# Kernel tuning notes

Measured on AMD Instinct MI355X. Metric: run time of the kernel, lower is better.

Reference implementation:

```python
import jax, jax.numpy as jnp
import numpy as np

B, D, P, C = 256, 2048, 8192, 8
N_CLUSTERS = P // C
MOMENTUM, TEMP = 0.2, 0.07
NEG_INF = jnp.float32(-1e30)


def setup_inputs() -> dict:
    key = jax.random.key(0)
    k1, k2, k3 = jax.random.split(key, 3)
    batch_feat = jax.random.normal(k1, (B, D), dtype=jnp.float32)
    batch_feat = batch_feat / jnp.linalg.norm(batch_feat, axis=1, keepdims=True)
    memory = jax.random.normal(k2, (P, D), dtype=jnp.float32)
    memory = memory / jnp.linalg.norm(memory, axis=1, keepdims=True)
    abs_proxy_label = jax.random.randint(k3, (B,), 0, P, dtype=jnp.int32)
    # each proxy is a (camera, cluster) pair: proxy p -> cam p % C, cluster p // C
    proxy_cam = (jnp.arange(P, dtype=jnp.int32) % C)
    proxy_cluster = (jnp.arange(P, dtype=jnp.int32) // C)
    camid = abs_proxy_label % C               # consistent with mapper[cam]
    pseudo_cluster_label = abs_proxy_label // C
    return dict(batch_feat=batch_feat, memory=memory,
                abs_proxy_label=abs_proxy_label, camid=camid,
                pseudo_cluster_label=pseudo_cluster_label,
                proxy_cam=proxy_cam, proxy_cluster=proxy_cluster,
                epoch=10, inter_loss_epoch=5, k=50)


def reference(batch_feat, memory, abs_proxy_label, camid, pseudo_cluster_label,
              proxy_cam, proxy_cluster, epoch, inter_loss_epoch, k):
    # ---------------- intra-camera proxy loss ----------------
    sim = (batch_feat @ memory.T) / TEMP                      # [B, P]
    cam_mask = camid[:, None] == proxy_cam[None, :]           # per-cam proxy subset
    logits = jnp.where(cam_mask, sim, NEG_INF)
    lse = jax.nn.logsumexp(logits, axis=1)
    tgt = jnp.take_along_axis(logits, abs_proxy_label[:, None].astype(jnp.int32), axis=1)[:, 0]
    ce = lse - tgt                                            # per-sample CE over its cam's proxies
    ones = jnp.ones((B,), dtype=jnp.float32)
    cam_counts = jax.ops.segment_sum(ones, camid, num_segments=C)
    ce_per_cam = jax.ops.segment_sum(ce, camid, num_segments=C)
    intra_loss = jnp.sum(jnp.where(cam_counts > 0, ce_per_cam / jnp.maximum(cam_counts, 1.0), 0.0))

    loss = intra_loss
    # ---------------- inter-camera loss ----------------
    if epoch >= inter_loss_epoch:
        sim_det = jax.lax.stop_gradient(batch_feat) @ memory.T     # kNN uses detached feat, no temp
        pos_mask = (proxy_cluster[None, :] == pseudo_cluster_label[:, None]) & \
                   (proxy_cam[None, :] != camid[:, None])          # same cluster, different cam
        neg_mask = proxy_cluster[None, :] != pseudo_cluster_label[:, None]  # inlier, different cluster
        neg_sim = jnp.where(neg_mask, sim_det, NEG_INF)
        thresh = jax.lax.top_k(neg_sim, k)[0][:, -1]               # drop k nearest negatives
        keep_neg = neg_mask & (sim_det < thresh[:, None])
        full_mask = pos_mask | keep_neg
        inter_logits = jnp.where(full_mask, sim, NEG_INF)
        logsm = inter_logits - jax.nn.logsumexp(inter_logits, axis=1, keepdims=True)
        pos_card = jnp.sum(pos_mask, axis=1).astype(jnp.float32)
        pos_sum = jnp.sum(jnp.where(pos_mask, logsm, 0.0), axis=1)
        loss_i = jnp.where(pos_card > 0, -pos_sum / jnp.maximum(pos_card, 1.0), 0.0)
        inter_per_cam = jax.ops.segment_sum(loss_i, camid, num_segments=C)
        loss = loss + jnp.sum(jnp.where(cam_counts > 0,
                                        0.5 * inter_per_cam / jnp.maximum(cam_counts, 1.0), 0.0))

    # ---------------- EMA memory-bank scatter update (torch does this in backward) ----------------
    def step(mem, xy):
        x, y = xy
        m = MOMENTUM * mem[y] + (1.0 - MOMENTUM) * x
        m = m / jnp.linalg.norm(m)
        return mem.at[y].set(m), None
    new_memory, _ = jax.lax.scan(
        step, memory, (jax.lax.stop_gradient(batch_feat), abs_proxy_label))
    return loss, new_memory
```

## Files before the change

### kernel.cpp

```cpp
#include <hip/hip_runtime.h>
#include <cstdint>

#define NB 256
#define ND 2048
#define NP 8192
#define NEG_INF_F (-1e30f)
#define INV_TEMP (1.0f/0.07f)

typedef __attribute__((ext_vector_type(8))) short          short8;
typedef __attribute__((ext_vector_type(8))) unsigned short ushort8;
typedef __attribute__((ext_vector_type(4))) float          floatx4;

__device__ __forceinline__ unsigned short f2bf(float f) {
  unsigned u = __float_as_uint(f);
  return (unsigned short)((u + 0x7fffu + ((u >> 16) & 1u)) >> 16);
}

__global__ __launch_bounds__(256)
void prep_kernel(const float* __restrict__ mem, const float* __restrict__ feat,
                 unsigned short* __restrict__ Mb, unsigned short* __restrict__ Fb,
                 float* __restrict__ memcopy ,
                 float* __restrict__ acc, unsigned* __restrict__ counter) {
  const int b = blockIdx.x, t = threadIdx.x;
  if (b < 8192) {
    const float4* src = (const float4*)(mem + (size_t)b * ND) + 2 * t;
    float4 a = src[0], c = src[1];
    ushort8 r;
    r[0]=f2bf(a.x); r[1]=f2bf(a.y); r[2]=f2bf(a.z); r[3]=f2bf(a.w);
    r[4]=f2bf(c.x); r[5]=f2bf(c.y); r[6]=f2bf(c.z); r[7]=f2bf(c.w);
    *(ushort8*)(Mb + (size_t)b * ND + 8 * t) = r;
    float* dst = memcopy + (size_t)b * ND + 8 * t;
    dst[0]=a.x; dst[1]=a.y; dst[2]=a.z; dst[3]=a.w;
    dst[4]=c.x; dst[5]=c.y; dst[6]=c.z; dst[7]=c.w;
  } else if (b < 8448) {
    const int i = (b - 8192) * 256 + t;
    const float4* src = (const float4*)feat + 2 * (size_t)i;
    float4 a = src[0], c = src[1];
    ushort8 r;
    r[0]=f2bf(a.x); r[1]=f2bf(a.y); r[2]=f2bf(a.z); r[3]=f2bf(a.w);
    r[4]=f2bf(c.x); r[5]=f2bf(c.y); r[6]=f2bf(c.z); r[7]=f2bf(c.w);
    *(ushort8*)(Fb + 8 * (size_t)i) = r;
  } else {
    if (t < 16) acc[t] = 0.f;
    if (t == 16) counter[0] = 0u;
  }
}

#define GLOAD_LDS16(g, l) __builtin_amdgcn_global_load_lds( \
  (const __attribute__((address_space(1))) unsigned int*)(g), \
  (__attribute__((address_space(3))) unsigned int*)(l), 16, 0, 0)

__global__ __launch_bounds__(256, 2)
void gemm_kernel(const unsigned short* __restrict__ Fb,
                 const unsigned short* __restrict__ Mb,
                 float* __restrict__ Sout) {
  __shared__ unsigned short sA[2][64 * 64];
  __shared__ unsigned short sB[2][128 * 64];
  const int tid  = threadIdx.x;
  const int wave = tid >> 6;
  const int lane = tid & 63;
  const int frow = lane & 15;
  const int kg   = lane >> 4;
  const int bn0  = blockIdx.x * 128;
  const int bm0  = blockIdx.y * 64;
  const size_t kofs = (size_t)blockIdx.z * 1024;

  const unsigned short* gA[2];
  #pragma unroll
  for (int q = 0; q < 2; ++q) {
    int c = q * 256 + tid, r = c >> 3, kc = (c & 7) ^ (r & 7);
    gA[q] = Fb + (size_t)(bm0 + r) * ND + kofs + kc * 8;
  }
  const unsigned short* gB[4];
  #pragma unroll
  for (int q = 0; q < 4; ++q) {
    int c = q * 256 + tid, r = c >> 3, kc = (c & 7) ^ (r & 7);
    gB[q] = Mb + (size_t)(bn0 + r) * ND + kofs + kc * 8;
  }
  const int ldsb = wave * 512;

  int offA[4][2], offB[2][2];
  #pragma unroll
  for (int m = 0; m < 4; ++m)
    #pragma unroll
    for (int kf = 0; kf < 2; ++kf) {
      int r = m * 16 + frow, sc = (kf * 4 + kg) ^ (r & 7);
      offA[m][kf] = r * 64 + sc * 8;
    }
  #pragma unroll
  for (int n = 0; n < 2; ++n)
    #pragma unroll
    for (int kf = 0; kf < 2; ++kf) {
      int r = wave * 32 + n * 16 + frow, sc = (kf * 4 + kg) ^ (r & 7);
      offB[n][kf] = r * 64 + sc * 8;
    }

  floatx4 acc[4][2];
  #pragma unroll
  for (int m = 0; m < 4; ++m)
    #pragma unroll
    for (int n = 0; n < 2; ++n)
      #pragma unroll
      for (int r = 0; r < 4; ++r) acc[m][n][r] = 0.f;

  auto stage = [&](int buf, int kt) {
    int kk = kt * 64;
    #pragma unroll
    for (int q = 0; q < 2; ++q) GLOAD_LDS16(gA[q] + kk, &sA[buf][q * 2048 + ldsb]);
    #pragma unroll
    for (int q = 0; q < 4; ++q) GLOAD_LDS16(gB[q] + kk, &sB[buf][q * 2048 + ldsb]);
  };
  auto compute = [&](int buf) {
    short8 af[4][2], bf[2][2];
    #pragma unroll
    for (int m = 0; m < 4; ++m)
      #pragma unroll
      for (int kf = 0; kf < 2; ++kf) af[m][kf] = *(const short8*)&sA[buf][offA[m][kf]];
    #pragma unroll
    for (int n = 0; n < 2; ++n)
      #pragma unroll
      for (int kf = 0; kf < 2; ++kf) bf[n][kf] = *(const short8*)&sB[buf][offB[n][kf]];
    #pragma unroll
    for (int m = 0; m < 4; ++m)
      #pragma unroll
      for (int n = 0; n < 2; ++n) {
        acc[m][n] = __builtin_amdgcn_mfma_f32_16x16x32_bf16(af[m][0], bf[n][0], acc[m][n], 0, 0, 0);
        acc[m][n] = __builtin_amdgcn_mfma_f32_16x16x32_bf16(af[m][1], bf[n][1], acc[m][n], 0, 0, 0);
      }
  };

  stage(0, 0);
  __syncthreads();
  int cur = 0;
  for (int kt = 0; kt < 15; ++kt) {
    stage(cur ^ 1, kt + 1);
    compute(cur);
    __syncthreads();
    cur ^= 1;
  }
  compute(cur);

  float* Sp = Sout + (size_t)blockIdx.z * ((size_t)NB * NP);
  #pragma unroll
  for (int m = 0; m < 4; ++m) {
    int row = bm0 + 16 * m + 4 * kg;
    #pragma unroll
    for (int n = 0; n < 2; ++n) {
      int col = bn0 + wave * 32 + 16 * n + frow;
      #pragma unroll
      for (int r = 0; r < 4; ++r)
        Sp[(size_t)(row + r) * NP + col] = acc[m][n][r];
    }
  }
}

__global__ __launch_bounds__(512)
void row_kernel(const float* __restrict__ S,
                const int* __restrict__ label,
                const int* __restrict__ camid,
                const int* __restrict__ pcl,
                const int* __restrict__ epoch_p,
                const int* __restrict__ ilep_p,
                const int* __restrict__ k_p,
                float* __restrict__ acc ,
                unsigned* __restrict__ counter,
                float* __restrict__ out) {
  __shared__ float red[2][3][8];
  __shared__ unsigned sh_done;
  __shared__ float cnt8[8], gsum[16];
  const int i = blockIdx.x, t = threadIdx.x, w = t >> 6;
  const bool l0 = (t & 63) == 0;
  int ph = 0;

  auto bmax = [&](float x) -> float {
    #pragma unroll
    for (int o = 32; o; o >>= 1) x = fmaxf(x, __shfl_xor(x, o));
    if (l0) red[ph][0][w] = x;
    __syncthreads();
    float r = red[ph][0][t & 7];
    #pragma unroll
    for (int o = 4; o; o >>= 1) r = fmaxf(r, __shfl_xor(r, o));
    ph ^= 1;
    return r;
  };
  auto bsum2 = [&](float& x, float& y) {
    #pragma unroll
    for (int o = 32; o; o >>= 1) { x += __shfl_xor(x, o); y += __shfl_xor(y, o); }
    if (l0) { red[ph][0][w] = x; red[ph][1][w] = y; }
    __syncthreads();
    float rx = red[ph][0][t & 7], ry = red[ph][1][t & 7];
    #pragma unroll
    for (int o = 4; o; o >>= 1) { rx += __shfl_xor(rx, o); ry += __shfl_xor(ry, o); }
    ph ^= 1; x = rx; y = ry;
  };
  auto bsum3 = [&](float& x, float& y, float& z) {
    #pragma unroll
    for (int o = 32; o; o >>= 1) {
      x += __shfl_xor(x, o); y += __shfl_xor(y, o); z += __shfl_xor(z, o);
    }
    if (l0) { red[ph][0][w] = x; red[ph][1][w] = y; red[ph][2][w] = z; }
    __syncthreads();
    float rx = red[ph][0][t & 7], ry = red[ph][1][t & 7], rz = red[ph][2][t & 7];
    #pragma unroll
    for (int o = 4; o; o >>= 1) {
      rx += __shfl_xor(rx, o); ry += __shfl_xor(ry, o); rz += __shfl_xor(rz, o);
    }
    ph ^= 1; x = rx; y = ry; z = rz;
  };

  const float* r0 = S + (size_t)i * NP;
  const float* r1 = r0 + (size_t)NB * NP;
  float v[16];
  {
    const float4* a0 = (const float4*)(r0 + (t << 4));
    const float4* a1 = (const float4*)(r1 + (t << 4));
    #pragma unroll
    for (int q = 0; q < 4; ++q) {
      float4 x = a0[q], y = a1[q];
      v[4*q+0] = x.x + y.x; v[4*q+1] = x.y + y.y;
      v[4*q+2] = x.z + y.z; v[4*q+3] = x.w + y.w;
    }
  }
  const int camI = camid[i], clI = pcl[i], lab = label[i];
  const bool negL = (2 * t)     != clI;
  const bool negH = (2 * t + 1) != clI;

  float m1 = fmaxf(v[camI], v[camI + 8]);
  m1 = bmax(m1);
  float s1 = __expf((v[camI] - m1) * INV_TEMP) + __expf((v[camI + 8] - m1) * INV_TEMP);
  float tg = (t == (lab >> 4)) ? v[lab & 15] : 0.f;
  bsum2(s1, tg);
  const float ce_i = m1 * INV_TEMP + __logf(s1) - tg * INV_TEMP;

  float li = 0.f;
  const bool inter = epoch_p[0] >= ilep_p[0];
  if (inter) {
    const float kneg = (float)k_p[0];
    unsigned kk[16];
    #pragma unroll
    for (int j = 0; j < 16; ++j) {
      unsigned u = __float_as_uint(v[j]);
      kk[j] = (u & 0x80000000u) ? ~u : (u | 0x80000000u);
    }
    unsigned tstar = 0u;
    for (int b = 30; b >= 0; b -= 2) {
      const unsigned c1 = tstar | (1u << b);
      const unsigned c2 = tstar | (2u << b);
      const unsigned c3 = tstar | (3u << b);
      float n1 = 0.f, n2 = 0.f, n3 = 0.f;
      #pragma unroll
      for (int j = 0; j < 16; ++j) {
        const bool ng = (j < 8) ? negL : negH;
        if (ng) {
          n1 += (kk[j] >= c1) ? 1.f : 0.f;
          n2 += (kk[j] >= c2) ? 1.f : 0.f;
          n3 += (kk[j] >= c3) ? 1.f : 0.f;
        }
      }
      bsum3(n1, n2, n3);
      if (n2 >= kneg)      tstar = (n3 >= kneg) ? c3 : c2;
      else if (n1 >= kneg) tstar = c1;
    }
    const float thr = __uint_as_float((tstar & 0x80000000u) ? (tstar ^ 0x80000000u) : ~tstar);

    float m2 = NEG_INF_F;
    unsigned posm = 0u, selm = 0u;
    #pragma unroll
    for (int j = 0; j < 16; ++j) {
      const bool ng = (j < 8) ? negL : negH;
      const bool pos = (!ng) && ((j & 7) != camI);
      const bool sel = pos || (ng && (v[j] < thr));
      if (pos) posm |= 1u << j;
      if (sel) { selm |= 1u << j; m2 = fmaxf(m2, v[j]); }
    }
    m2 = bmax(m2);
    float s2 = 0.f, sp = 0.f, card = 0.f;
    #pragma unroll
    for (int j = 0; j < 16; ++j) {
      if ((selm >> j) & 1u) s2 += __expf((v[j] - m2) * INV_TEMP);
      if ((posm >> j) & 1u) { sp += v[j]; card += 1.f; }
    }
    bsum3(s2, sp, card);
    const float lse2 = m2 * INV_TEMP + __logf(s2);
    li = (card > 0.f) ? -(sp * INV_TEMP - card * lse2) / card : 0.f;
  }

  if (t == 0) {
    atomicAdd(&acc[camI], ce_i);
    atomicAdd(&acc[8 + camI], li);
    __threadfence();
    sh_done = atomicAdd(counter, 1u);
  }
  __syncthreads();
  if (sh_done == NB - 1) {
    if (t < 8) cnt8[t] = 0.f;
    __syncthreads();
    if (t < NB) atomicAdd(&cnt8[camid[t]], 1.f);
    if (t < 16) gsum[t] = acc[t];
    __syncthreads();
    if (t == 0) {
      float l = 0.f;
      for (int c = 0; c < 8; ++c)
        if (cnt8[c] > 0.f) {
          l += gsum[c] / cnt8[c];
          if (inter) l += 0.5f * gsum[8 + c] / cnt8[c];
        }
      out[0] = l;
    }
  }
}

__global__ __launch_bounds__(256)
void ema_kernel(const float* __restrict__ feat,
                const float* __restrict__ mem,
                const int* __restrict__ label,
                float* __restrict__ outmem) {
  __shared__ float red[4];
  __shared__ int slab[NB];
  const int b = blockIdx.x, t = threadIdx.x;
  slab[t] = label[t];
  __syncthreads();
  const int y = slab[b];
  bool mine = true;
  for (int j = 0; j < b; ++j)
    if (slab[j] == y) { mine = false; break; }
  if (!mine) return;
  float m[8];
  #pragma unroll
  for (int q = 0; q < 8; ++q) m[q] = mem[(size_t)y * ND + q * 256 + t];
  for (int i = b; i < NB; ++i) {
    if (slab[i] != y) continue;
    float ss = 0.f;
    #pragma unroll
    for (int q = 0; q < 8; ++q) {
      m[q] = 0.2f * m[q] + 0.8f * feat[(size_t)i * ND + q * 256 + t];
      ss += m[q] * m[q];
    }
    #pragma unroll
    for (int o = 32; o; o >>= 1) ss += __shfl_xor(ss, o);
    if ((t & 63) == 0) red[t >> 6] = ss;
    __syncthreads();
    ss = red[0] + red[1] + red[2] + red[3];
    __syncthreads();
    float inv = 1.f / sqrtf(ss);
    #pragma unroll
    for (int q = 0; q < 8; ++q) m[q] *= inv;
  }
  #pragma unroll
  for (int q = 0; q < 8; ++q) outmem[(size_t)y * ND + q * 256 + t] = m[q];
}

extern "C" void kernel_launch(void* const* d_in, const int* in_sizes, int n_in,
                              void* d_out, int out_size, void* d_ws, size_t ws_size,
                              hipStream_t stream) {
  const float* feat = (const float*)d_in[0];
  const float* mem  = (const float*)d_in[1];
  const int* lab    = (const int*)d_in[2];
  const int* cam    = (const int*)d_in[3];
  const int* pcl    = (const int*)d_in[4];
  const int* ep     = (const int*)d_in[7];
  const int* ilep   = (const int*)d_in[8];
  const int* kp     = (const int*)d_in[9];
  float* out = (float*)d_out;

  char* ws = (char*)d_ws;
  unsigned short* Mb = (unsigned short*)(ws);
  unsigned short* Fb = (unsigned short*)(ws + 33554432);
  float*          S  = (float*)(ws + 34603008);
  float*          acc = (float*)(ws + 51380224);
  unsigned*       ctr = (unsigned*)(ws + 51380224 + 64);

  prep_kernel<<<8449, 256, 0, stream>>>(mem, feat, Mb, Fb, out + 1, acc, ctr);
  gemm_kernel<<<dim3(NP / 128, NB / 64, 2), 256, 0, stream>>>(Fb, Mb, S);
  row_kernel<<<NB, 512, 0, stream>>>(S, lab, cam, pcl, ep, ilep, kp, acc, ctr, out);
  ema_kernel<<<NB, 256, 0, stream>>>(feat, mem, lab, out + 1);
}
```

Before: 219.3 us.

## Use radix-histogram top-k threshold and aligned float4 memory copy stores

The per-row k-th-largest negative threshold search changes from a 16-round, 2-bit-per-round counting search with block reductions to a 4-round, 8-bit radix select. Each round builds a 256-bin shared-memory histogram with atomics and finds the target bucket with a wavefront suffix scan. Separately, the prep kernel stages each memory row in LDS and writes the copy to out+1 as 16-byte aligned float4 stores. This replaces scalar stores that were misaligned by the one-float output offset. Costs are shared-memory atomic contention in the histogram and extra barriers in prep.

After: 202.4 us. -7.7%, faster.

```diff
diff --git a/kernel.cpp b/kernel.cpp
--- a/kernel.cpp
+++ b/kernel.cpp
@@ -19,8 +19,9 @@
 __global__ __launch_bounds__(256)
 void prep_kernel(const float* __restrict__ mem, const float* __restrict__ feat,
                  unsigned short* __restrict__ Mb, unsigned short* __restrict__ Fb,
-                 float* __restrict__ memcopy ,
+                 float* __restrict__ out ,
                  float* __restrict__ acc, unsigned* __restrict__ counter) {
+  __shared__ float row[ND];
   const int b = blockIdx.x, t = threadIdx.x;
   if (b < 8192) {
     const float4* src = (const float4*)(mem + (size_t)b * ND) + 2 * t;
@@ -29,9 +30,25 @@
     r[0]=f2bf(a.x); r[1]=f2bf(a.y); r[2]=f2bf(a.z); r[3]=f2bf(a.w);
     r[4]=f2bf(c.x); r[5]=f2bf(c.y); r[6]=f2bf(c.z); r[7]=f2bf(c.w);
     *(ushort8*)(Mb + (size_t)b * ND + 8 * t) = r;
-    float* dst = memcopy + (size_t)b * ND + 8 * t;
-    dst[0]=a.x; dst[1]=a.y; dst[2]=a.z; dst[3]=a.w;
-    dst[4]=c.x; dst[5]=c.y; dst[6]=c.z; dst[7]=c.w;
+    *(float4*)(row + 8 * t)     = a;
+    *(float4*)(row + 8 * t + 4) = c;
+    __syncthreads();
+    float* dst = out + 1 + (size_t)b * ND;
+    {
+      int q = t;
+      float4 lo = *(const float4*)(row + 4 * q);
+      float4 hi = *(const float4*)(row + 4 * q + 4);
+      float4 w = {lo.w, hi.x, hi.y, hi.z};
+      *(float4*)(dst + 4 * q + 3) = w;
+    }
+    if (t < 255) {
+      int q = t + 256;
+      float4 lo = *(const float4*)(row + 4 * q);
+      float4 hi = *(const float4*)(row + 4 * q + 4);
+      float4 w = {lo.w, hi.x, hi.y, hi.z};
+      *(float4*)(dst + 4 * q + 3) = w;
+    }
+    if (t == 0) { dst[0]=row[0]; dst[1]=row[1]; dst[2]=row[2]; dst[2047]=row[2047]; }
   } else if (b < 8448) {
     const int i = (b - 8192) * 256 + t;
     const float4* src = (const float4*)feat + 2 * (size_t)i;
@@ -166,6 +183,8 @@
                 unsigned* __restrict__ counter,
                 float* __restrict__ out) {
   __shared__ float red[2][3][8];
+  __shared__ unsigned hist[256];
+  __shared__ unsigned bc_d, bc_k;
   __shared__ unsigned sh_done;
   __shared__ float cnt8[8], gsum[16];
   const int i = blockIdx.x, t = threadIdx.x, w = t >> 6;
@@ -235,32 +254,59 @@
   float li = 0.f;
   const bool inter = epoch_p[0] >= ilep_p[0];
   if (inter) {
-    const float kneg = (float)k_p[0];
     unsigned kk[16];
     #pragma unroll
     for (int j = 0; j < 16; ++j) {
       unsigned u = __float_as_uint(v[j]);
       kk[j] = (u & 0x80000000u) ? ~u : (u | 0x80000000u);
     }
-    unsigned tstar = 0u;
-    for (int b = 30; b >= 0; b -= 2) {
-      const unsigned c1 = tstar | (1u << b);
-      const unsigned c2 = tstar | (2u << b);
-      const unsigned c3 = tstar | (3u << b);
-      float n1 = 0.f, n2 = 0.f, n3 = 0.f;
-      #pragma unroll
-      for (int j = 0; j < 16; ++j) {
-        const bool ng = (j < 8) ? negL : negH;
-        if (ng) {
-          n1 += (kk[j] >= c1) ? 1.f : 0.f;
-          n2 += (kk[j] >= c2) ? 1.f : 0.f;
-          n3 += (kk[j] >= c3) ? 1.f : 0.f;
+    unsigned prefix = 0u, krem = (unsigned)k_p[0];
+    #pragma unroll
+    for (int round = 0; round < 4; ++round) {
+      const int sh = 24 - 8 * round;
+      if (t < 256) hist[t] = 0u;
+      __syncthreads();
+      if (round == 0) {
+        #pragma unroll
+        for (int j = 0; j < 16; ++j) {
+          const bool ng = (j < 8) ? negL : negH;
+          if (ng) atomicAdd(&hist[kk[j] >> 24], 1u);
+        }
+      } else {
+        #pragma unroll
+        for (int j = 0; j < 16; ++j) {
+          const bool ng = (j < 8) ? negL : negH;
+          if (ng && ((kk[j] >> (sh + 8)) == (prefix >> (sh + 8))))
+            atomicAdd(&hist[(kk[j] >> sh) & 255u], 1u);
         }
       }
-      bsum3(n1, n2, n3);
-      if (n2 >= kneg)      tstar = (n3 >= kneg) ? c3 : c2;
-      else if (n1 >= kneg) tstar = c1;
-    }
+      __syncthreads();
+      if (t < 64) {
+        unsigned h0 = hist[4*t], h1 = hist[4*t+1], h2 = hist[4*t+2], h3 = hist[4*t+3];
+        unsigned s = h0 + h1 + h2 + h3;
+        unsigned suf = s;
+        #pragma unroll
+        for (int o = 1; o < 64; o <<= 1) {
+          unsigned g = __shfl_down(suf, o);
+          if (t + o < 64) suf += g;
+        }
+        const unsigned above = suf - s;
+        const unsigned ge3 = above + h3, ge2 = ge3 + h2, ge1 = ge2 + h1, ge0 = ge1 + h0;
+        int dsel = -1; unsigned sub = 0u;
+        if      (ge3 >= krem && above < krem) { dsel = 3; sub = above; }
+        else if (ge2 >= krem && ge3  < krem) { dsel = 2; sub = ge3; }
+        else if (ge1 >= krem && ge2  < krem) { dsel = 1; sub = ge2; }
+        else if (ge0 >= krem && ge1  < krem) { dsel = 0; sub = ge1; }
+        if (dsel >= 0) {
+          bc_d = (unsigned)(4 * t + dsel);
+          bc_k = krem - sub;
+        }
+      }
+      __syncthreads();
+      prefix |= bc_d << sh;
+      krem = bc_k;
+    }
+    const unsigned tstar = prefix;
     const float thr = __uint_as_float((tstar & 0x80000000u) ? (tstar ^ 0x80000000u) : ~tstar);
 
     float m2 = NEG_INF_F;
@@ -370,7 +416,7 @@
   float*          acc = (float*)(ws + 51380224);
   unsigned*       ctr = (unsigned*)(ws + 51380224 + 64);
 
-  prep_kernel<<<8449, 256, 0, stream>>>(mem, feat, Mb, Fb, out + 1, acc, ctr);
+  prep_kernel<<<8449, 256, 0, stream>>>(mem, feat, Mb, Fb, out, acc, ctr);
   gemm_kernel<<<dim3(NP / 128, NB / 64, 2), 256, 0, stream>>>(Fb, Mb, S);
   row_kernel<<<NB, 512, 0, stream>>>(S, lab, cam, pcl, ep, ilep, kp, acc, ctr, out);
   ema_kernel<<<NB, 256, 0, stream>>>(feat, mem, lab, out + 1);
```
